# Kernel optimization log

Measured on AMD Instinct MI355X. Metric: run time of the kernel, lower is better.

## Reference

```python
import jax, jax.numpy as jnp
import numpy as np

N_NODES = 100000
N_EDGES = 1600000
N_IN = 8
N_PRE = 32
C = 128
N_LAYERS = 8


def _lin(key, fan_in, fan_out):
    kw, kb = jax.random.split(key)
    s = 1.0 / np.sqrt(fan_in).astype(np.float32)
    W = jax.random.uniform(kw, (fan_in, fan_out), minval=-s, maxval=s, dtype=jnp.float32)
    b = jax.random.uniform(kb, (fan_out,), minval=-s, maxval=s, dtype=jnp.float32)
    return W, b


def setup_inputs() -> dict:
    key = jax.random.key(0)
    ks = jax.random.split(key, 9)
    x = jax.random.normal(ks[0], (N_NODES, N_IN), dtype=jnp.float32)
    edge_index = jax.random.randint(ks[1], (2, N_EDGES), 0, N_NODES, dtype=jnp.int32)
    Wp, bp = _lin(ks[2], N_IN, N_PRE)      # preproc
    W1, b1 = _lin(ks[3], N_PRE, C)         # fc_input_1 (node_identity)
    W2, b2 = _lin(ks[4], N_PRE, C)         # fc_input_2
    Wg, bg = _lin(ks[5], C, C)             # tied GCNConv weight/bias
    Wd, bd = _lin(ks[6], 2 * C, C)         # tied dense fusion
    Wf1, bf1 = _lin(ks[7], 2 * C, C)       # final_fc1
    Wf2, bf2 = _lin(ks[8], C, 2)           # final_fc2
    return {"x": x, "edge_index": edge_index, "Wp": Wp, "bp": bp, "W1": W1, "b1": b1,
            "W2": W2, "b2": b2, "Wg": Wg, "bg": bg, "Wd": Wd, "bd": bd,
            "Wf1": Wf1, "bf1": bf1, "Wf2": Wf2, "bf2": bf2}


def _gcn(h, Wg, bg, src, dst):
    # PyG GCNConv: add self-loops, norm = deg^-1/2[src] * deg^-1/2[dst].
    # Norm factorizes, so scale at node level instead of per edge.
    hw = h @ Wg                                                  # [N, C]
    deg = jnp.zeros((N_NODES,), jnp.float32).at[dst].add(1.0) + 1.0  # +1 self-loop
    dis = jax.lax.rsqrt(deg)                                     # deg^-1/2
    hs = hw * dis[:, None]
    agg = jax.ops.segment_sum(hs[src], dst, num_segments=N_NODES)
    return (agg + hs) * dis[:, None] + bg                        # hs term = self-loop (deg^-1 * hw)


def reference(x, edge_index, Wp, bp, W1, b1, W2, b2, Wg, bg, Wd, bd, Wf1, bf1, Wf2, bf2):
    src, dst = edge_index[0], edge_index[1]
    h0 = x @ Wp + bp                       # preproc_activation = none
    ni = jax.nn.relu(h0 @ W1 + b1)         # node_identity
    h = jax.nn.relu(h0 @ W2 + b2)
    for _ in range(N_LAYERS):              # tied gnn layers; dropout is identity (inference)
        g = jax.nn.relu(_gcn(h, Wg, bg, src, dst))
        h = jax.nn.relu(jnp.concatenate([ni, g], axis=1) @ Wd + bd)
    h = jax.nn.relu(jnp.concatenate([ni, h], axis=1) @ Wf1 + bf1)
    return h @ Wf2 + bf2                   # output_activation never applied in forward
```

## Files before the change

kernel.cpp:

```cpp
#include <hip/hip_runtime.h>

#define N_NODES 100000
#define N_EDGES 1600000
#define NB 391
#define NTASK (N_NODES / 16)

typedef unsigned short ushort_t;
typedef __attribute__((ext_vector_type(8))) short bf16x8;
typedef __attribute__((ext_vector_type(4))) float f32x4;

__device__ __forceinline__ float bf2f(unsigned short u) {
    union { unsigned u; float f; } x; x.u = ((unsigned)u) << 16; return x.f;
}
__device__ __forceinline__ unsigned short f2bf(float f) {
    union { float f; unsigned u; } x; x.f = f;
    unsigned r = x.u + 0x7fffu + ((x.u >> 16) & 1u);
    return (unsigned short)(r >> 16);
}

__global__ void k_zero(unsigned* p, int n) {
    int i = blockIdx.x * 256 + threadIdx.x;
    if (i < n) p[i] = 0u;
}

__global__ void k_deg(const int* __restrict__ dst, unsigned* __restrict__ cnt) {
    int e = blockIdx.x * 256 + threadIdx.x;
    if (e < N_EDGES) atomicAdd(&cnt[dst[e]], 1u);
}

__global__ void k_dis(const unsigned* __restrict__ cnt, float* __restrict__ dis,
                      float* __restrict__ sdeg) {
    int i = blockIdx.x * 256 + threadIdx.x;
    if (i < N_NODES) {
        float d = (float)cnt[i] + 1.0f;
        float s = sqrtf(d);
        sdeg[i] = s;
        dis[i] = 1.0f / s;
    }
}

__global__ void __launch_bounds__(256) k_bsum(const unsigned* __restrict__ cnt,
                                              unsigned* __restrict__ bsum) {
    __shared__ unsigned sh[256];
    int i = blockIdx.x * 256 + threadIdx.x;
    sh[threadIdx.x] = (i < N_NODES) ? cnt[i] : 0u;
    __syncthreads();
    for (int off = 128; off > 0; off >>= 1) {
        if (threadIdx.x < off) sh[threadIdx.x] += sh[threadIdx.x + off];
        __syncthreads();
    }
    if (threadIdx.x == 0) bsum[blockIdx.x] = sh[0];
}

__global__ void __launch_bounds__(512) k_bscan(unsigned* __restrict__ bsum) {
    __shared__ unsigned sh[512];
    int t = threadIdx.x;
    unsigned v = (t < NB) ? bsum[t] : 0u;
    sh[t] = v;
    __syncthreads();
    for (int off = 1; off < 512; off <<= 1) {
        unsigned u = (t >= off) ? sh[t - off] : 0u;
        __syncthreads();
        sh[t] += u;
        __syncthreads();
    }
    if (t < NB) bsum[t] = sh[t] - v;
}

__global__ void __launch_bounds__(256) k_apply(const unsigned* __restrict__ cnt,
                                               const unsigned* __restrict__ bsum,
                                               unsigned* __restrict__ row_ptr,
                                               unsigned* __restrict__ cur) {
    __shared__ unsigned sh[256];
    int i = blockIdx.x * 256 + threadIdx.x;
    int t = threadIdx.x;
    unsigned v = (i < N_NODES) ? cnt[i] : 0u;
    sh[t] = v;
    __syncthreads();
    for (int off = 1; off < 256; off <<= 1) {
        unsigned u = (t >= off) ? sh[t - off] : 0u;
        __syncthreads();
        sh[t] += u;
        __syncthreads();
    }
    if (i < N_NODES) {
        row_ptr[i] = bsum[blockIdx.x] + sh[t] - v;
        cur[i] = 0u;
    }
    if (i == N_NODES - 1) row_ptr[N_NODES] = N_EDGES;
}

__global__ void k_fill(const int* __restrict__ src, const int* __restrict__ dst,
                       const unsigned* __restrict__ row_ptr, unsigned* __restrict__ cur,
                       unsigned* __restrict__ col) {
    int e = blockIdx.x * 256 + threadIdx.x;
    if (e < N_EDGES) {
        int d = dst[e];
        unsigned pos = row_ptr[d] + atomicAdd(&cur[d], 1u);
        col[pos] = (unsigned)src[e];
    }
}

__global__ void k_tr(const float* __restrict__ Wd, const float* __restrict__ Wf1,
                     const float* __restrict__ Wg, ushort_t* __restrict__ WT) {
    const float* srcs[5] = {Wd, Wf1, Wg, Wd + 128 * 128, Wf1 + 128 * 128};
    const float* S = srcs[blockIdx.x];
    ushort_t* Dhi = WT + (size_t)(2 * blockIdx.x) * 16384;
    ushort_t* Dlo = Dhi + 16384;
    for (int i = threadIdx.x; i < 128 * 128; i += blockDim.x) {
        int n = i >> 7, k = i & 127;
        float w = S[k * 128 + n];
        unsigned short h = f2bf(w);
        Dhi[n * 128 + k] = h;
        Dlo[n * 128 + k] = f2bf(w - bf2f(h));
    }
}

__global__ void __launch_bounds__(128) k_pre1(
    const float* __restrict__ x, const float* __restrict__ Wp,
    const float* __restrict__ bp, const float* __restrict__ W1,
    const float* __restrict__ b1, const float* __restrict__ W2,
    const float* __restrict__ b2, const float* __restrict__ dis,
    float* __restrict__ ni, ushort_t* __restrict__ hd) {
    __shared__ float h0s[4][32];
    int j = threadIdx.x;
    long n0 = (long)blockIdx.x * 4;
    {
        int nn = j >> 5, c = j & 31;
        float acc = bp[c];
#pragma unroll
        for (int k = 0; k < 8; ++k)
            acc += x[(n0 + nn) * 8 + k] * Wp[k * 32 + c];
        h0s[nn][c] = acc;
    }
    __syncthreads();
    float ni_a[4], h1_a[4];
    float bb1 = b1[j], bb2 = b2[j];
#pragma unroll
    for (int m = 0; m < 4; ++m) { ni_a[m] = bb1; h1_a[m] = bb2; }
    for (int cc = 0; cc < 32; ++cc) {
        float w1 = W1[cc * 128 + j];
        float w2 = W2[cc * 128 + j];
#pragma unroll
        for (int m = 0; m < 4; ++m) {
            float h0v = h0s[m][cc];
            ni_a[m] += h0v * w1;
            h1_a[m] += h0v * w2;
        }
    }
#pragma unroll
    for (int m = 0; m < 4; ++m) {
        long node = n0 + m;
        ni[node * 128 + j] = fmaxf(ni_a[m], 0.f);
        hd[node * 128 + j] = f2bf(fmaxf(h1_a[m], 0.f) * dis[node]);
    }
}

__device__ __forceinline__ void load_split_frags(const float* __restrict__ p,
                                                 bf16x8* ahi, bf16x8* alo) {
#pragma unroll
    for (int kc = 0; kc < 4; ++kc) {
        const float* q = p + kc * 32;
#pragma unroll
        for (int j = 0; j < 8; ++j) {
            float f = q[j];
            unsigned short h = f2bf(f);
            ahi[kc][j] = (short)h;
            alo[kc][j] = (short)f2bf(f - bf2f(h));
        }
    }
}

__device__ __forceinline__ void mfma_tiles(const bf16x8* ahi, const bf16x8* alo,
                                           const ushort_t* __restrict__ WThi,
                                           const ushort_t* __restrict__ WTlo,
                                           int r16, int q, f32x4* acc) {
#pragma unroll
    for (int t = 0; t < 8; ++t) {
        const ushort_t* bh = WThi + (t * 16 + r16) * 128 + q * 8;
        const ushort_t* bl = WTlo + (t * 16 + r16) * 128 + q * 8;
#pragma unroll
        for (int kc = 0; kc < 4; ++kc) {
            bf16x8 bhv = *(const bf16x8*)(bh + kc * 32);
            bf16x8 blv = *(const bf16x8*)(bl + kc * 32);
            acc[t] = __builtin_amdgcn_mfma_f32_16x16x32_bf16(alo[kc], bhv, acc[t], 0, 0, 0);
            acc[t] = __builtin_amdgcn_mfma_f32_16x16x32_bf16(ahi[kc], blv, acc[t], 0, 0, 0);
            acc[t] = __builtin_amdgcn_mfma_f32_16x16x32_bf16(ahi[kc], bhv, acc[t], 0, 0, 0);
        }
    }
}

__global__ void __launch_bounds__(256) gemm_bias(
    const float* __restrict__ in, const ushort_t* __restrict__ WThi,
    const ushort_t* __restrict__ WTlo, const float* __restrict__ bias,
    ushort_t* __restrict__ out) {
    int task = blockIdx.x * 4 + (threadIdx.x >> 6);
    if (task >= NTASK) return;
    int lane = threadIdx.x & 63;
    int q = lane >> 4, r16 = lane & 15;
    long base = (long)task * 16;

    bf16x8 ahi[4], alo[4];
    load_split_frags(in + (base + r16) * 128 + q * 8, ahi, alo);

    f32x4 acc[8];
#pragma unroll
    for (int t = 0; t < 8; ++t) acc[t] = {0.f, 0.f, 0.f, 0.f};
    mfma_tiles(ahi, alo, WThi, WTlo, r16, q, acc);

#pragma unroll
    for (int t = 0; t < 8; ++t) {
        int n = t * 16 + r16;
        float bv = bias[n];
#pragma unroll
        for (int r = 0; r < 4; ++r) {
            long node = base + q * 4 + r;
            out[node * 128 + n] = f2bf(acc[t][r] + bv);
        }
    }
}

__device__ __forceinline__ void acc8(uint4 w, float* a) {
    a[0] += __uint_as_float(w.x << 16);
    a[1] += __uint_as_float(w.x & 0xffff0000u);
    a[2] += __uint_as_float(w.y << 16);
    a[3] += __uint_as_float(w.y & 0xffff0000u);
    a[4] += __uint_as_float(w.z << 16);
    a[5] += __uint_as_float(w.z & 0xffff0000u);
    a[6] += __uint_as_float(w.w << 16);
    a[7] += __uint_as_float(w.w & 0xffff0000u);
}

__global__ void __launch_bounds__(256, 4) k_fused(
    const unsigned* __restrict__ rowp, const unsigned* __restrict__ col,
    const ushort_t* __restrict__ hd_in,
    const ushort_t* __restrict__ hi_wg, const ushort_t* __restrict__ lo_wg,
    const float* __restrict__ bg,
    const ushort_t* __restrict__ hi_wd, const ushort_t* __restrict__ lo_wd,
    const ushort_t* __restrict__ niWd, const float* __restrict__ dis,
    ushort_t* __restrict__ hd_out) {
    __shared__ float gsh[4][16 * 132];
    int wid = threadIdx.x >> 6;
    int lane = threadIdx.x & 63;
    int task = blockIdx.x * 4 + wid;
    if (task >= NTASK) return;
    long base = (long)task * 16;
    float* gw = gsh[wid];
    const uint4* h4 = (const uint4*)hd_in;

    int g = lane >> 4;
    int l = lane & 15;

#pragma unroll 1
    for (int i = 0; i < 4; ++i) {
        int m = g * 4 + i;
        long node = base + m;
        unsigned b = rowp[node], e = rowp[node + 1];
        uint4 own = h4[node * 16 + l];
        float a[8] = {0.f, 0.f, 0.f, 0.f, 0.f, 0.f, 0.f, 0.f};
        acc8(own, a);
        unsigned t = b;
        for (; t + 4 <= e; t += 4) {
            unsigned s0 = col[t], s1 = col[t + 1], s2 = col[t + 2], s3 = col[t + 3];
            uint4 w0 = h4[(long)s0 * 16 + l];
            uint4 w1 = h4[(long)s1 * 16 + l];
            uint4 w2 = h4[(long)s2 * 16 + l];
            uint4 w3 = h4[(long)s3 * 16 + l];
            acc8(w0, a); acc8(w1, a); acc8(w2, a); acc8(w3, a);
        }
        for (; t < e; ++t) {
            uint4 w = h4[(long)col[t] * 16 + l];
            acc8(w, a);
        }
        float* dst = gw + m * 132 + 8 * l;
        *(float4*)dst = make_float4(a[0], a[1], a[2], a[3]);
        *(float4*)(dst + 4) = make_float4(a[4], a[5], a[6], a[7]);
    }

    int q = lane >> 4, r16 = lane & 15;
    bf16x8 ahi[4], alo[4];
    load_split_frags(gw + r16 * 132 + q * 8, ahi, alo);

    f32x4 acc[8];
#pragma unroll
    for (int t = 0; t < 8; ++t) acc[t] = {0.f, 0.f, 0.f, 0.f};
    mfma_tiles(ahi, alo, hi_wg, lo_wg, r16, q, acc);

    float sc[4];
#pragma unroll
    for (int r = 0; r < 4; ++r) sc[r] = dis[base + q * 4 + r];

#pragma unroll
    for (int t = 0; t < 8; ++t) {
        int n = t * 16 + r16;
        float bv = bg[n];
#pragma unroll
        for (int r = 0; r < 4; ++r) {
            int m = q * 4 + r;
            gw[m * 132 + n] = fmaxf(acc[t][r] * sc[r] + bv, 0.f);
        }
    }

    load_split_frags(gw + r16 * 132 + q * 8, ahi, alo);
#pragma unroll
    for (int t = 0; t < 8; ++t) acc[t] = {0.f, 0.f, 0.f, 0.f};
    mfma_tiles(ahi, alo, hi_wd, lo_wd, r16, q, acc);

#pragma unroll
    for (int t = 0; t < 8; ++t) {
        int n = t * 16 + r16;
#pragma unroll
        for (int r = 0; r < 4; ++r) {
            long node = base + q * 4 + r;
            float nv = bf2f(niWd[node * 128 + n]);
            hd_out[node * 128 + n] = f2bf(fmaxf(acc[t][r] + nv, 0.f) * sc[r]);
        }
    }
}

__global__ void __launch_bounds__(256) k_fin(
    const ushort_t* __restrict__ in, const ushort_t* __restrict__ WThi,
    const ushort_t* __restrict__ WTlo, const ushort_t* __restrict__ niWf,
    const float* __restrict__ sdeg, float* __restrict__ out) {
    int task = blockIdx.x * 4 + (threadIdx.x >> 6);
    if (task >= NTASK) return;
    int lane = threadIdx.x & 63;
    int q = lane >> 4, r16 = lane & 15;
    long base = (long)task * 16;

    bf16x8 a[4];
    const ushort_t* arow = in + (base + r16) * 128 + q * 8;
#pragma unroll
    for (int kc = 0; kc < 4; ++kc) a[kc] = *(const bf16x8*)(arow + kc * 32);

    f32x4 acc[8];
#pragma unroll
    for (int t = 0; t < 8; ++t) acc[t] = {0.f, 0.f, 0.f, 0.f};
#pragma unroll
    for (int t = 0; t < 8; ++t) {
        const ushort_t* bh = WThi + (t * 16 + r16) * 128 + q * 8;
        const ushort_t* bl = WTlo + (t * 16 + r16) * 128 + q * 8;
#pragma unroll
        for (int kc = 0; kc < 4; ++kc) {
            bf16x8 bhv = *(const bf16x8*)(bh + kc * 32);
            bf16x8 blv = *(const bf16x8*)(bl + kc * 32);
            acc[t] = __builtin_amdgcn_mfma_f32_16x16x32_bf16(a[kc], blv, acc[t], 0, 0, 0);
            acc[t] = __builtin_amdgcn_mfma_f32_16x16x32_bf16(a[kc], bhv, acc[t], 0, 0, 0);
        }
    }

    float sc[4];
#pragma unroll
    for (int r = 0; r < 4; ++r) sc[r] = sdeg[base + q * 4 + r];
#pragma unroll
    for (int t = 0; t < 8; ++t) {
        int n = t * 16 + r16;
#pragma unroll
        for (int r = 0; r < 4; ++r) {
            long node = base + q * 4 + r;
            float nv = bf2f(niWf[node * 128 + n]);
            out[node * 128 + n] = fmaxf(acc[t][r] * sc[r] + nv, 0.f);
        }
    }
}

__global__ void __launch_bounds__(256) k_fc2(const float* __restrict__ hf,
                                             const float* __restrict__ Wf2,
                                             const float* __restrict__ bf2v,
                                             float* __restrict__ out) {
    int node = blockIdx.x * 4 + (threadIdx.x >> 6);
    if (node >= N_NODES) return;
    int lane = threadIdx.x & 63;
    float2 hv = ((const float2*)hf)[(long)node * 64 + lane];
    float4 wv = *(const float4*)(Wf2 + lane * 4);
    float p0 = hv.x * wv.x + hv.y * wv.z;
    float p1 = hv.x * wv.y + hv.y * wv.w;
    for (int o = 32; o > 0; o >>= 1) {
        p0 += __shfl_down(p0, o, 64);
        p1 += __shfl_down(p1, o, 64);
    }
    if (lane == 0) {
        float2 r; r.x = p0 + bf2v[0]; r.y = p1 + bf2v[1];
        ((float2*)out)[node] = r;
    }
}

extern "C" void kernel_launch(void* const* d_in, const int* in_sizes, int n_in,
                              void* d_out, int out_size, void* d_ws, size_t ws_size,
                              hipStream_t stream) {
    const float* x    = (const float*)d_in[0];
    const int* ei     = (const int*)d_in[1];
    const float* Wp   = (const float*)d_in[2];
    const float* bp   = (const float*)d_in[3];
    const float* W1   = (const float*)d_in[4];
    const float* b1   = (const float*)d_in[5];
    const float* W2   = (const float*)d_in[6];
    const float* b2   = (const float*)d_in[7];
    const float* Wg   = (const float*)d_in[8];
    const float* bg   = (const float*)d_in[9];
    const float* Wd   = (const float*)d_in[10];
    const float* bd   = (const float*)d_in[11];
    const float* Wf1  = (const float*)d_in[12];
    const float* bf1  = (const float*)d_in[13];
    const float* Wf2  = (const float*)d_in[14];
    const float* bf2v = (const float*)d_in[15];

    char* w = (char*)d_ws;
    auto carve = [&](size_t bytes) {
        void* p = (void*)w;
        w += (bytes + 255) & ~(size_t)255;
        return p;
    };
    float* dis      = (float*)carve((size_t)N_NODES * 4);
    float* sdeg     = (float*)carve((size_t)N_NODES * 4);
    unsigned* cnt   = (unsigned*)carve((size_t)N_NODES * 4);
    unsigned* bsum  = (unsigned*)carve((size_t)NB * 4);
    unsigned* rowp  = (unsigned*)carve((size_t)(N_NODES + 1) * 4);
    unsigned* col   = (unsigned*)carve((size_t)N_EDGES * 4);
    ushort_t* hdA   = (ushort_t*)carve((size_t)N_NODES * 128 * 2);
    ushort_t* hdB   = (ushort_t*)carve((size_t)N_NODES * 128 * 2);
    float* gbuf     = (float*)carve((size_t)N_NODES * 128 * 4);
    ushort_t* niWd  = (ushort_t*)carve((size_t)N_NODES * 128 * 2);
    ushort_t* niWf  = (ushort_t*)carve((size_t)N_NODES * 128 * 2);
    ushort_t* WT    = (ushort_t*)carve((size_t)10 * 16384 * 2);
    ushort_t* hi_wdtop  = WT + 0 * 16384; ushort_t* lo_wdtop  = WT + 1 * 16384;
    ushort_t* hi_wf1top = WT + 2 * 16384; ushort_t* lo_wf1top = WT + 3 * 16384;
    ushort_t* hi_wg     = WT + 4 * 16384; ushort_t* lo_wg     = WT + 5 * 16384;
    ushort_t* hi_wdbot  = WT + 6 * 16384; ushort_t* lo_wdbot  = WT + 7 * 16384;
    ushort_t* hi_wf1bot = WT + 8 * 16384; ushort_t* lo_wf1bot = WT + 9 * 16384;

    const int* srcp = ei;
    const int* dstp = ei + N_EDGES;

    const int GE = (N_EDGES + 255) / 256;
    const int GN = (N_NODES + 255) / 256;
    const int GW = (N_NODES + 3) / 4;
    const int GG = (NTASK + 3) / 4;

    k_zero<<<GN, 256, 0, stream>>>(cnt, N_NODES);
    k_deg<<<GE, 256, 0, stream>>>(dstp, cnt);
    k_dis<<<GN, 256, 0, stream>>>(cnt, dis, sdeg);
    k_bsum<<<NB, 256, 0, stream>>>(cnt, bsum);
    k_bscan<<<1, 512, 0, stream>>>(bsum);
    k_apply<<<NB, 256, 0, stream>>>(cnt, bsum, rowp, cnt);
    k_fill<<<GE, 256, 0, stream>>>(srcp, dstp, rowp, cnt, col);
    k_tr<<<5, 256, 0, stream>>>(Wd, Wf1, Wg, WT);
    k_pre1<<<N_NODES / 4, 128, 0, stream>>>(x, Wp, bp, W1, b1, W2, b2, dis, gbuf, hdA);
    gemm_bias<<<GG, 256, 0, stream>>>(gbuf, hi_wdtop, lo_wdtop, bd, niWd);
    gemm_bias<<<GG, 256, 0, stream>>>(gbuf, hi_wf1top, lo_wf1top, bf1, niWf);
    ushort_t* hin = hdA;
    ushort_t* hout = hdB;
    for (int l = 0; l < 8; ++l) {
        k_fused<<<GG, 256, 0, stream>>>(rowp, col, hin, hi_wg, lo_wg, bg,
                                        hi_wdbot, lo_wdbot, niWd, dis, hout);
        ushort_t* tmp = hin; hin = hout; hout = tmp;
    }
    k_fin<<<GG, 256, 0, stream>>>(hin, hi_wf1bot, lo_wf1bot, niWf, sdeg, gbuf);
    k_fc2<<<GW, 256, 0, stream>>>(gbuf, Wf2, bf2v, (float*)d_out);
}
```

Before: 1.801 ms.

## Pad CSR rows to multiples of eight and double-buffer neighbor gathers

Each node's adjacency list is padded to a multiple of 8 entries. The padding slots point at a dummy zero row appended to each feature buffer, so the aggregation loop can load column indices as uint4 pairs and issue 8-wide gathers with software double-buffering, with no scalar remainder loop. The node-identity input is also stored as bf16, so the two initial GEMMs drop the hi/lo split of the activation and run two MFMAs per step instead of three. The trade-offs are extra padding traffic, a fill pass over the index buffer, lower occupancy (launch bound 3) and reduced precision on the node-identity path.

```diff
diff --git a/kernel.cpp b/kernel.cpp
--- a/kernel.cpp
+++ b/kernel.cpp
@@ -4,6 +4,7 @@
 #define N_EDGES 1600000
 #define NB 391
 #define NTASK (N_NODES / 16)
+#define COLPAD (N_EDGES + 7 * N_NODES + 64)
 
 typedef unsigned short ushort_t;
 typedef __attribute__((ext_vector_type(8))) short bf16x8;
@@ -21,6 +22,11 @@
 __global__ void k_zero(unsigned* p, int n) {
     int i = blockIdx.x * 256 + threadIdx.x;
     if (i < n) p[i] = 0u;
+}
+
+__global__ void k_filld(unsigned* p) {
+    int i = blockIdx.x * 256 + threadIdx.x;
+    if (i < COLPAD) p[i] = (unsigned)N_NODES;
 }
 
 __global__ void k_deg(const int* __restrict__ dst, unsigned* __restrict__ cnt) {
@@ -43,7 +49,7 @@
                                               unsigned* __restrict__ bsum) {
     __shared__ unsigned sh[256];
     int i = blockIdx.x * 256 + threadIdx.x;
-    sh[threadIdx.x] = (i < N_NODES) ? cnt[i] : 0u;
+    sh[threadIdx.x] = (i < N_NODES) ? ((cnt[i] + 7u) & ~7u) : 0u;
     __syncthreads();
     for (int off = 128; off > 0; off >>= 1) {
         if (threadIdx.x < off) sh[threadIdx.x] += sh[threadIdx.x + off];
@@ -69,12 +75,12 @@
 
 __global__ void __launch_bounds__(256) k_apply(const unsigned* __restrict__ cnt,
                                                const unsigned* __restrict__ bsum,
-                                               unsigned* __restrict__ row_ptr,
+                                               unsigned* __restrict__ prow,
                                                unsigned* __restrict__ cur) {
     __shared__ unsigned sh[256];
     int i = blockIdx.x * 256 + threadIdx.x;
     int t = threadIdx.x;
-    unsigned v = (i < N_NODES) ? cnt[i] : 0u;
+    unsigned v = (i < N_NODES) ? ((cnt[i] + 7u) & ~7u) : 0u;
     sh[t] = v;
     __syncthreads();
     for (int off = 1; off < 256; off <<= 1) {
@@ -84,21 +90,27 @@
         __syncthreads();
     }
     if (i < N_NODES) {
-        row_ptr[i] = bsum[blockIdx.x] + sh[t] - v;
+        prow[i] = bsum[blockIdx.x] + sh[t] - v;
         cur[i] = 0u;
     }
-    if (i == N_NODES - 1) row_ptr[N_NODES] = N_EDGES;
+    if (i == N_NODES - 1) prow[N_NODES] = bsum[blockIdx.x] + sh[t];
 }
 
 __global__ void k_fill(const int* __restrict__ src, const int* __restrict__ dst,
-                       const unsigned* __restrict__ row_ptr, unsigned* __restrict__ cur,
-                       unsigned* __restrict__ col) {
+                       const unsigned* __restrict__ prow, unsigned* __restrict__ cur,
+                       unsigned* __restrict__ colp) {
     int e = blockIdx.x * 256 + threadIdx.x;
     if (e < N_EDGES) {
         int d = dst[e];
-        unsigned pos = row_ptr[d] + atomicAdd(&cur[d], 1u);
-        col[pos] = (unsigned)src[e];
-    }
+        unsigned pos = prow[d] + atomicAdd(&cur[d], 1u);
+        colp[pos] = (unsigned)src[e];
+    }
+}
+
+__global__ void k_dummy(ushort_t* hdA, ushort_t* hdB) {
+    int t = threadIdx.x;
+    if (t < 128) hdA[(size_t)N_NODES * 128 + t] = 0;
+    else hdB[(size_t)N_NODES * 128 + (t - 128)] = 0;
 }
 
 __global__ void k_tr(const float* __restrict__ Wd, const float* __restrict__ Wf1,
@@ -121,7 +133,7 @@
     const float* __restrict__ bp, const float* __restrict__ W1,
     const float* __restrict__ b1, const float* __restrict__ W2,
     const float* __restrict__ b2, const float* __restrict__ dis,
-    float* __restrict__ ni, ushort_t* __restrict__ hd) {
+    ushort_t* __restrict__ ni, ushort_t* __restrict__ hd) {
     __shared__ float h0s[4][32];
     int j = threadIdx.x;
     long n0 = (long)blockIdx.x * 4;
@@ -151,7 +163,7 @@
 #pragma unroll
     for (int m = 0; m < 4; ++m) {
         long node = n0 + m;
-        ni[node * 128 + j] = fmaxf(ni_a[m], 0.f);
+        ni[node * 128 + j] = f2bf(fmaxf(ni_a[m], 0.f));
         hd[node * 128 + j] = f2bf(fmaxf(h1_a[m], 0.f) * dis[node]);
     }
 }
@@ -191,7 +203,7 @@
 }
 
 __global__ void __launch_bounds__(256) gemm_bias(
-    const float* __restrict__ in, const ushort_t* __restrict__ WThi,
+    const ushort_t* __restrict__ in, const ushort_t* __restrict__ WThi,
     const ushort_t* __restrict__ WTlo, const float* __restrict__ bias,
     ushort_t* __restrict__ out) {
     int task = blockIdx.x * 4 + (threadIdx.x >> 6);
@@ -200,14 +212,26 @@
     int q = lane >> 4, r16 = lane & 15;
     long base = (long)task * 16;
 
-    bf16x8 ahi[4], alo[4];
-    load_split_frags(in + (base + r16) * 128 + q * 8, ahi, alo);
+    bf16x8 a[4];
+    const ushort_t* arow = in + (base + r16) * 128 + q * 8;
+#pragma unroll
+    for (int kc = 0; kc < 4; ++kc) a[kc] = *(const bf16x8*)(arow + kc * 32);
 
     f32x4 acc[8];
 #pragma unroll
     for (int t = 0; t < 8; ++t) acc[t] = {0.f, 0.f, 0.f, 0.f};
-    mfma_tiles(ahi, alo, WThi, WTlo, r16, q, acc);
-
+#pragma unroll
+    for (int t = 0; t < 8; ++t) {
+        const ushort_t* bh = WThi + (t * 16 + r16) * 128 + q * 8;
+        const ushort_t* bl = WTlo + (t * 16 + r16) * 128 + q * 8;
+#pragma unroll
+        for (int kc = 0; kc < 4; ++kc) {
+            bf16x8 bhv = *(const bf16x8*)(bh + kc * 32);
+            bf16x8 blv = *(const bf16x8*)(bl + kc * 32);
+            acc[t] = __builtin_amdgcn_mfma_f32_16x16x32_bf16(a[kc], blv, acc[t], 0, 0, 0);
+            acc[t] = __builtin_amdgcn_mfma_f32_16x16x32_bf16(a[kc], bhv, acc[t], 0, 0, 0);
+        }
+    }
 #pragma unroll
     for (int t = 0; t < 8; ++t) {
         int n = t * 16 + r16;
@@ -231,8 +255,25 @@
     a[7] += __uint_as_float(w.w & 0xffff0000u);
 }
 
-__global__ void __launch_bounds__(256, 4) k_fused(
-    const unsigned* __restrict__ rowp, const unsigned* __restrict__ col,
+__device__ __forceinline__ void gather8(uint4* G, uint4 c0, uint4 c1,
+                                        const uint4* __restrict__ h4, int l) {
+    G[0] = h4[(long)c0.x * 16 + l];
+    G[1] = h4[(long)c0.y * 16 + l];
+    G[2] = h4[(long)c0.z * 16 + l];
+    G[3] = h4[(long)c0.w * 16 + l];
+    G[4] = h4[(long)c1.x * 16 + l];
+    G[5] = h4[(long)c1.y * 16 + l];
+    G[6] = h4[(long)c1.z * 16 + l];
+    G[7] = h4[(long)c1.w * 16 + l];
+}
+
+__device__ __forceinline__ void accbatch(const uint4* G, float* a) {
+#pragma unroll
+    for (int j = 0; j < 8; ++j) acc8(G[j], a);
+}
+
+__global__ void __launch_bounds__(256, 3) k_fused(
+    const unsigned* __restrict__ prow, const unsigned* __restrict__ colp,
     const ushort_t* __restrict__ hd_in,
     const ushort_t* __restrict__ hi_wg, const ushort_t* __restrict__ lo_wg,
     const float* __restrict__ bg,
@@ -255,26 +296,39 @@
     for (int i = 0; i < 4; ++i) {
         int m = g * 4 + i;
         long node = base + m;
-        unsigned b = rowp[node], e = rowp[node + 1];
+        float a[8] = {0.f, 0.f, 0.f, 0.f, 0.f, 0.f, 0.f, 0.f};
         uint4 own = h4[node * 16 + l];
-        float a[8] = {0.f, 0.f, 0.f, 0.f, 0.f, 0.f, 0.f, 0.f};
+        unsigned t0 = prow[node];
+        int nb = (int)((prow[node + 1] - t0) >> 3);
         acc8(own, a);
-        unsigned t = b;
-        for (; t + 4 <= e; t += 4) {
-            unsigned s0 = col[t], s1 = col[t + 1], s2 = col[t + 2], s3 = col[t + 3];
-            uint4 w0 = h4[(long)s0 * 16 + l];
-            uint4 w1 = h4[(long)s1 * 16 + l];
-            uint4 w2 = h4[(long)s2 * 16 + l];
-            uint4 w3 = h4[(long)s3 * 16 + l];
-            acc8(w0, a); acc8(w1, a); acc8(w2, a); acc8(w3, a);
-        }
-        for (; t < e; ++t) {
-            uint4 w = h4[(long)col[t] * 16 + l];
-            acc8(w, a);
-        }
-        float* dst = gw + m * 132 + 8 * l;
-        *(float4*)dst = make_float4(a[0], a[1], a[2], a[3]);
-        *(float4*)(dst + 4) = make_float4(a[4], a[5], a[6], a[7]);
+        if (nb > 0) {
+            const uint4* cp = (const uint4*)(colp + t0);
+            uint4 cX0 = cp[0], cX1 = cp[1];
+            uint4 cY0 = cp[2], cY1 = cp[3];
+            cp += 4;
+            uint4 GA[8], GB[8];
+            gather8(GA, cX0, cX1, h4, l);
+            int k = 0;
+            for (; k + 2 < nb; k += 2) {
+                cX0 = cp[0]; cX1 = cp[1];
+                gather8(GB, cY0, cY1, h4, l);
+                accbatch(GA, a);
+                cY0 = cp[2]; cY1 = cp[3];
+                cp += 4;
+                gather8(GA, cX0, cX1, h4, l);
+                accbatch(GB, a);
+            }
+            if (nb - k == 2) {
+                gather8(GB, cY0, cY1, h4, l);
+                accbatch(GA, a);
+                accbatch(GB, a);
+            } else {
+                accbatch(GA, a);
+            }
+        }
+        float* dstp = gw + m * 132 + 8 * l;
+        *(float4*)dstp = make_float4(a[0], a[1], a[2], a[3]);
+        *(float4*)(dstp + 4) = make_float4(a[4], a[5], a[6], a[7]);
     }
 
     int q = lane >> 4, r16 = lane & 15;
@@ -415,11 +469,12 @@
     float* sdeg     = (float*)carve((size_t)N_NODES * 4);
     unsigned* cnt   = (unsigned*)carve((size_t)N_NODES * 4);
     unsigned* bsum  = (unsigned*)carve((size_t)NB * 4);
-    unsigned* rowp  = (unsigned*)carve((size_t)(N_NODES + 1) * 4);
-    unsigned* col   = (unsigned*)carve((size_t)N_EDGES * 4);
-    ushort_t* hdA   = (ushort_t*)carve((size_t)N_NODES * 128 * 2);
-    ushort_t* hdB   = (ushort_t*)carve((size_t)N_NODES * 128 * 2);
-    float* gbuf     = (float*)carve((size_t)N_NODES * 128 * 4);
+    unsigned* prow  = (unsigned*)carve((size_t)(N_NODES + 1) * 4);
+    unsigned* colp  = (unsigned*)carve((size_t)COLPAD * 4);
+    ushort_t* hdA   = (ushort_t*)carve((size_t)(N_NODES + 1) * 128 * 2);
+    ushort_t* hdB   = (ushort_t*)carve((size_t)(N_NODES + 1) * 128 * 2);
+    ushort_t* niB   = (ushort_t*)carve((size_t)N_NODES * 128 * 2);
+    float* hf       = (float*)carve((size_t)N_NODES * 128 * 4);
     ushort_t* niWd  = (ushort_t*)carve((size_t)N_NODES * 128 * 2);
     ushort_t* niWf  = (ushort_t*)carve((size_t)N_NODES * 128 * 2);
     ushort_t* WT    = (ushort_t*)carve((size_t)10 * 16384 * 2);
@@ -434,27 +489,30 @@
 
     const int GE = (N_EDGES + 255) / 256;
     const int GN = (N_NODES + 255) / 256;
+    const int GP = (COLPAD + 255) / 256;
     const int GW = (N_NODES + 3) / 4;
     const int GG = (NTASK + 3) / 4;
 
     k_zero<<<GN, 256, 0, stream>>>(cnt, N_NODES);
+    k_filld<<<GP, 256, 0, stream>>>(colp);
     k_deg<<<GE, 256, 0, stream>>>(dstp, cnt);
     k_dis<<<GN, 256, 0, stream>>>(cnt, dis, sdeg);
     k_bsum<<<NB, 256, 0, stream>>>(cnt, bsum);
     k_bscan<<<1, 512, 0, stream>>>(bsum);
-    k_apply<<<NB, 256, 0, stream>>>(cnt, bsum, rowp, cnt);
-    k_fill<<<GE, 256, 0, stream>>>(srcp, dstp, rowp, cnt, col);
+    k_apply<<<NB, 256, 0, stream>>>(cnt, bsum, prow, cnt);
+    k_fill<<<GE, 256, 0, stream>>>(srcp, dstp, prow, cnt, colp);
+    k_dummy<<<1, 256, 0, stream>>>(hdA, hdB);
     k_tr<<<5, 256, 0, stream>>>(Wd, Wf1, Wg, WT);
-    k_pre1<<<N_NODES / 4, 128, 0, stream>>>(x, Wp, bp, W1, b1, W2, b2, dis, gbuf, hdA);
-    gemm_bias<<<GG, 256, 0, stream>>>(gbuf, hi_wdtop, lo_wdtop, bd, niWd);
-    gemm_bias<<<GG, 256, 0, stream>>>(gbuf, hi_wf1top, lo_wf1top, bf1, niWf);
+    k_pre1<<<N_NODES / 4, 128, 0, stream>>>(x, Wp, bp, W1, b1, W2, b2, dis, niB, hdA);
+    gemm_bias<<<GG, 256, 0, stream>>>(niB, hi_wdtop, lo_wdtop, bd, niWd);
+    gemm_bias<<<GG, 256, 0, stream>>>(niB, hi_wf1top, lo_wf1top, bf1, niWf);
     ushort_t* hin = hdA;
     ushort_t* hout = hdB;
     for (int l = 0; l < 8; ++l) {
-        k_fused<<<GG, 256, 0, stream>>>(rowp, col, hin, hi_wg, lo_wg, bg,
+        k_fused<<<GG, 256, 0, stream>>>(prow, colp, hin, hi_wg, lo_wg, bg,
                                         hi_wdbot, lo_wdbot, niWd, dis, hout);
         ushort_t* tmp = hin; hin = hout; hout = tmp;
     }
-    k_fin<<<GG, 256, 0, stream>>>(hin, hi_wf1bot, lo_wf1bot, niWf, sdeg, gbuf);
-    k_fc2<<<GW, 256, 0, stream>>>(gbuf, Wf2, bf2v, (float*)d_out);
-}
+    k_fin<<<GG, 256, 0, stream>>>(hin, hi_wf1bot, lo_wf1bot, niWf, sdeg, hf);
+    k_fc2<<<GW, 256, 0, stream>>>(hf, Wf2, bf2v, (float*)d_out);
+}
```

Measured after the change: 1.776 ms. No clear change (-1.4%).
